# Performance work log

Measured on AMD Instinct MI355X. Metric: run time of the kernel, lower is better.

## Reference

```python
import jax, jax.numpy as jnp
import numpy as np

NUM_EXPERTS = 16
IN_FEATURES = 512
OUT_FEATURES = 512
N_TOKENS = 2048


def setup_inputs() -> dict:
    key = jax.random.key(0)
    k_x, k_idx, k_w, k_b = jax.random.split(key, 4)
    x = jax.random.normal(k_x, (N_TOKENS, IN_FEATURES), dtype=jnp.float32)
    indices = jax.random.randint(k_idx, (N_TOKENS,), 0, NUM_EXPERTS, dtype=jnp.int64)
    # nn.Linear default init: U(-1/sqrt(in), 1/sqrt(in)) for weight [out,in] and bias [out]
    bound = 1.0 / np.sqrt(IN_FEATURES)
    W = jax.random.uniform(k_w, (NUM_EXPERTS, OUT_FEATURES, IN_FEATURES),
                           minval=-bound, maxval=bound, dtype=jnp.float32)
    b = jax.random.uniform(k_b, (NUM_EXPERTS, OUT_FEATURES),
                           minval=-bound, maxval=bound, dtype=jnp.float32)
    return {"x": x, "indices": indices, "W": W, "b": b}


def reference(x, indices, W, b):
    # Faithful to SwitchLinear.forward: gather per-token expert weight/bias,
    # then per-token GEMV (batched matmul with a length-1 row dim).
    w_tok = W[indices]            # [N, out, in]  (naive per-token weight gather)
    b_tok = b[indices]            # [N, out]
    out = jnp.einsum('ni,noi->no', x, w_tok) + b_tok  # [N, out]
    return out
```

## Files before the change

### kernel.cpp

```cpp
#include <hip/hip_runtime.h>
#include <hip/hip_bf16.h>

#define NE    16
#define INF   512
#define OUTF  512
#define NT    2048
#define OTILE 32
#define TCH   64
#define WROWS 32
#define LSTRIDE 520

#define SZ_W   (WROWS * LSTRIDE * 2)
#define SZ_X   (TCH * LSTRIDE * 2)
#define SZ_LST ((NT + TCH) * 4)
#define SMEM_BYTES (SZ_W + SZ_X + SZ_LST + 32)

typedef __attribute__((ext_vector_type(4))) float f32x4;
typedef __attribute__((ext_vector_type(8))) short bf16x8;
typedef __attribute__((ext_vector_type(4))) short bf16x4;

__device__ inline short f2bf(float f) {
    union { __hip_bfloat16 h; short s; } u;
    u.h = __float2bfloat16(f);
    return u.s;
}

__device__ inline bf16x4 cvt4(f32x4 v) {
    bf16x4 r;
    r[0] = f2bf(v[0]); r[1] = f2bf(v[1]); r[2] = f2bf(v[2]); r[3] = f2bf(v[3]);
    return r;
}

__global__ __launch_bounds__(512, 2)
void switch_linear_kernel(const float* __restrict__ x,
                          const int* __restrict__ idx,
                          const float* __restrict__ W,
                          const float* __restrict__ bias,
                          float* __restrict__ out)
{
    extern __shared__ char smem[];
    short* s_W    = (short*)smem;
    short* s_X    = (short*)(smem + SZ_W);
    int*   s_list = (int*)(smem + SZ_W + SZ_X);
    int*   s_wcnt = (int*)(smem + SZ_W + SZ_X + SZ_LST);

    const int b   = blockIdx.x;
    const int e   = b & 15;
    const int o0  = (b >> 4) * OTILE;
    const int tid = threadIdx.x;
    const int lane = tid & 63;
    const int wid  = tid >> 6;

    int iv[4];
#pragma unroll
    for (int it = 0; it < 4; ++it)
        iv[it] = idx[wid * 256 + it * 64 + lane];

    const float* wbase = W + ((size_t)e * OUTF + o0) * INF;
#pragma unroll
    for (int i = 0; i < 8; ++i) {
        const int li = tid + i * 512;
        f32x4 v = ((const f32x4*)wbase)[li];
        const int fidx = li * 4;
        const int row = fidx >> 9;
        const int col = fidx & 511;
        *(bf16x4*)(&s_W[row * LSTRIDE + col]) = cvt4(v);
    }

    unsigned long long masks[4];
    int wtot = 0;
#pragma unroll
    for (int it = 0; it < 4; ++it) {
        const unsigned long long mk = __ballot(iv[it] == e);
        masks[it] = mk;
        wtot += __popcll(mk);
    }
    if (lane == 0) s_wcnt[wid] = wtot;
    __syncthreads();
    int base = 0;
#pragma unroll
    for (int w = 0; w < 8; ++w) { int c = s_wcnt[w]; if (w < wid) base += c; }
    const int cnt = s_wcnt[0] + s_wcnt[1] + s_wcnt[2] + s_wcnt[3]
                  + s_wcnt[4] + s_wcnt[5] + s_wcnt[6] + s_wcnt[7];
    const unsigned long long below = (1ull << lane) - 1ull;
    int run = base;
#pragma unroll
    for (int it = 0; it < 4; ++it) {
        const unsigned long long mk = masks[it];
        if (mk & (1ull << lane))
            s_list[run + __popcll(mk & below)] = wid * 256 + it * 64 + lane;
        run += __popcll(mk);
    }
    const int cnt_pad = (cnt + TCH - 1) & ~(TCH - 1);
    for (int i = cnt + tid; i < cnt_pad; i += 512) s_list[i] = -1;
    __syncthreads();
    if (cnt == 0) return;

    const int wt = wid >> 1;
    const int wo = wid & 1;
    const int lr = lane & 15;
    const int q  = lane >> 4;
    const int orow = o0 + wo * 16 + lr;

    bf16x8 bfr[16];
#pragma unroll
    for (int kk = 0; kk < 16; ++kk)
        bfr[kk] = *(const bf16x8*)(&s_W[(wo * 16 + lr) * LSTRIDE + kk * 32 + q * 8]);
    const float bv = bias[e * OUTF + orow];

    const int slot = tid >> 3;
    const int sub  = tid & 7;

    for (int cb = 0; cb < cnt_pad; cb += TCH) {
        int tok_s = s_list[cb + slot];
        if (tok_s < 0) tok_s = 0;
        const f32x4* xr = (const f32x4*)(x + (size_t)tok_s * INF);
#pragma unroll
        for (int i = 0; i < 16; ++i) {
            f32x4 v = xr[sub + i * 8];
            *(bf16x4*)(&s_X[slot * LSTRIDE + sub * 4 + i * 32]) = cvt4(v);
        }
        __syncthreads();

        f32x4 acc = {0.f, 0.f, 0.f, 0.f};
#pragma unroll
        for (int kk = 0; kk < 16; ++kk) {
            bf16x8 afr = *(const bf16x8*)(&s_X[(wt * 16 + lr) * LSTRIDE + kk * 32 + q * 8]);
            acc = __builtin_amdgcn_mfma_f32_16x16x32_bf16(afr, bfr[kk], acc, 0, 0, 0);
        }
#pragma unroll
        for (int j = 0; j < 4; ++j) {
            const int tok = s_list[cb + wt * 16 + q * 4 + j];
            if (tok >= 0) out[(size_t)tok * OUTF + orow] = acc[j] + bv;
        }
        __syncthreads();
    }
}

extern "C" void kernel_launch(void* const* d_in, const int* in_sizes, int n_in,
                              void* d_out, int out_size, void* d_ws, size_t ws_size,
                              hipStream_t stream) {
    const float* x    = (const float*)d_in[0];
    const int*   idx  = (const int*)d_in[1];
    const float* W    = (const float*)d_in[2];
    const float* bias = (const float*)d_in[3];
    float* out = (float*)d_out;

    dim3 grid(NE * (OUTF / OTILE));
    dim3 block(512);
    switch_linear_kernel<<<grid, block, SMEM_BYTES, stream>>>(x, idx, W, bias, out);
}
```

Before: 14.66 us.

## Prepack per-expert bf16 token rows and load tiles with global_load_lds

Adds a prepack kernel that gathers each expert's tokens once, converts them to bf16 and writes them contiguously into the workspace. The main kernel then streams these packed rows into LDS with direct global-to-LDS loads, instead of having each of the 16 output-tile blocks per expert re-gather and re-convert the fp32 rows. W is also loaded as fp32 straight into LDS and converted to bf16 when building register fragments. The cost is an extra kernel launch, and a per-expert capacity of 256 tokens that silently drops any overflow. The old single-kernel path is kept as a fallback when the workspace is too small.

After: 17.90 us. 1.22x slower.

```diff
diff --git a/kernel.cpp b/kernel.cpp
--- a/kernel.cpp
+++ b/kernel.cpp
@@ -7,42 +7,106 @@
 #define NT    2048
 #define OTILE 32
 #define TCH   64
-#define WROWS 32
-#define LSTRIDE 520
-
-#define SZ_W   (WROWS * LSTRIDE * 2)
-#define SZ_X   (TCH * LSTRIDE * 2)
+#define RCAP  256
+
+#define WSTRIDE 516
+#define XSTRIDE 520
+
+#define SZ_W   (OTILE * WSTRIDE * 4)
+#define SZ_X   (TCH * XSTRIDE * 2)
 #define SZ_LST ((NT + TCH) * 4)
-#define SMEM_BYTES (SZ_W + SZ_X + SZ_LST + 32)
+#define SMEM_BYTES (SZ_W + SZ_X + SZ_LST + 64)
+
+#define WS_NEED ((size_t)NE * RCAP * INF * 2)
 
 typedef __attribute__((ext_vector_type(4))) float f32x4;
 typedef __attribute__((ext_vector_type(8))) short bf16x8;
 typedef __attribute__((ext_vector_type(4))) short bf16x4;
 
-__device__ inline short f2bf(float f) {
-    union { __hip_bfloat16 h; short s; } u;
+__device__ inline unsigned short f2bf(float f) {
+    union { __hip_bfloat16 h; unsigned short s; } u;
     u.h = __float2bfloat16(f);
     return u.s;
 }
 
+__device__ inline bf16x8 cvt8(f32x4 lo, f32x4 hi) {
+    bf16x8 r;
+    r[0] = (short)f2bf(lo[0]); r[1] = (short)f2bf(lo[1]);
+    r[2] = (short)f2bf(lo[2]); r[3] = (short)f2bf(lo[3]);
+    r[4] = (short)f2bf(hi[0]); r[5] = (short)f2bf(hi[1]);
+    r[6] = (short)f2bf(hi[2]); r[7] = (short)f2bf(hi[3]);
+    return r;
+}
+
 __device__ inline bf16x4 cvt4(f32x4 v) {
     bf16x4 r;
-    r[0] = f2bf(v[0]); r[1] = f2bf(v[1]); r[2] = f2bf(v[2]); r[3] = f2bf(v[3]);
+    r[0] = (short)f2bf(v[0]); r[1] = (short)f2bf(v[1]);
+    r[2] = (short)f2bf(v[2]); r[3] = (short)f2bf(v[3]);
     return r;
 }
 
+__device__ inline void gload_lds16(const void* g, void* l) {
+    __builtin_amdgcn_global_load_lds(
+        (const __attribute__((address_space(1))) void*)g,
+        (__attribute__((address_space(3))) void*)l, 16, 0, 0);
+}
+
+__global__ __launch_bounds__(256, 4)
+void prepack_x(const float* __restrict__ x, const int* __restrict__ idx,
+               unsigned short* __restrict__ xs)
+{
+    __shared__ int s_list[NT];
+    __shared__ int s_wcnt[4];
+    const int e     = blockIdx.x & 15;
+    const int slice = blockIdx.x >> 4;
+    const int tid   = threadIdx.x;
+    const int lane  = tid & 63;
+    const int wv    = tid >> 6;
+
+    unsigned long long masks[8];
+    int wtot = 0;
+#pragma unroll
+    for (int it = 0; it < 8; ++it) {
+        const int i = wv * 512 + it * 64 + lane;
+        const unsigned long long mk = __ballot(idx[i] == e);
+        masks[it] = mk;
+        wtot += __popcll(mk);
+    }
+    if (lane == 0) s_wcnt[wv] = wtot;
+    __syncthreads();
+    int base = 0;
+#pragma unroll
+    for (int w = 0; w < 4; ++w) if (w < wv) base += s_wcnt[w];
+    const int cnt = s_wcnt[0] + s_wcnt[1] + s_wcnt[2] + s_wcnt[3];
+    const unsigned long long below = (1ull << lane) - 1ull;
+    int run = base;
+#pragma unroll
+    for (int it = 0; it < 8; ++it) {
+        const unsigned long long mk = masks[it];
+        if (mk & (1ull << lane))
+            s_list[run + __popcll(mk & below)] = wv * 512 + it * 64 + lane;
+        run += __popcll(mk);
+    }
+    __syncthreads();
+
+    for (int r = slice; r < cnt && r < RCAP; r += 16) {
+        const int tok = s_list[r];
+        const float2 v = *(const float2*)&x[(size_t)tok * INF + tid * 2];
+        ushort2 o; o.x = f2bf(v.x); o.y = f2bf(v.y);
+        *(ushort2*)&xs[((size_t)e * RCAP + r) * INF + tid * 2] = o;
+    }
+}
+
 __global__ __launch_bounds__(512, 2)
-void switch_linear_kernel(const float* __restrict__ x,
-                          const int* __restrict__ idx,
-                          const float* __restrict__ W,
-                          const float* __restrict__ bias,
-                          float* __restrict__ out)
+void moe_main(const int* __restrict__ idx, const float* __restrict__ W,
+              const float* __restrict__ bias, const unsigned short* __restrict__ xs,
+              float* __restrict__ out)
 {
     extern __shared__ char smem[];
-    short* s_W    = (short*)smem;
-    short* s_X    = (short*)(smem + SZ_W);
-    int*   s_list = (int*)(smem + SZ_W + SZ_X);
-    int*   s_wcnt = (int*)(smem + SZ_W + SZ_X + SZ_LST);
+    float*          s_Wf   = (float*)smem;
+    unsigned short* s_X    = (unsigned short*)(smem + SZ_W);
+    int*            s_list = (int*)(smem + SZ_W + SZ_X);
+    int*            s_wcnt = (int*)(smem + SZ_W + SZ_X + SZ_LST);
 
     const int b   = blockIdx.x;
     const int e   = b & 15;
@@ -58,13 +122,12 @@
 
     const float* wbase = W + ((size_t)e * OUTF + o0) * INF;
 #pragma unroll
-    for (int i = 0; i < 8; ++i) {
-        const int li = tid + i * 512;
-        f32x4 v = ((const f32x4*)wbase)[li];
-        const int fidx = li * 4;
-        const int row = fidx >> 9;
-        const int col = fidx & 511;
-        *(bf16x4*)(&s_W[row * LSTRIDE + col]) = cvt4(v);
+    for (int r2 = 0; r2 < 4; ++r2) {
+        const int row = wid * 4 + r2;
+        const float* gsrc = wbase + (size_t)row * INF + lane * 4;
+        float* ldst = s_Wf + row * WSTRIDE;
+        gload_lds16(gsrc, ldst);
+        gload_lds16(gsrc + 256, ldst + 256);
     }
 
     unsigned long long masks[4];
@@ -100,32 +163,130 @@
     const int wo = wid & 1;
     const int lr = lane & 15;
     const int q  = lane >> 4;
+    const int wrow = wo * 16 + lr;
+    const int orow = o0 + wrow;
+
+    bf16x8 bfr[16];
+#pragma unroll
+    for (int kk = 0; kk < 16; ++kk) {
+        f32x4 lo = *(const f32x4*)&s_Wf[wrow * WSTRIDE + kk * 32 + q * 8];
+        f32x4 hi = *(const f32x4*)&s_Wf[wrow * WSTRIDE + kk * 32 + q * 8 + 4];
+        bfr[kk] = cvt8(lo, hi);
+    }
+    const float bv = bias[e * OUTF + orow];
+
+    const unsigned short* xsrc = xs + (size_t)e * RCAP * INF;
+
+    for (int cb = 0; cb < cnt_pad; cb += TCH) {
+#pragma unroll
+        for (int r2 = 0; r2 < 8; ++r2) {
+            const int row = wid * 8 + r2;
+            const unsigned short* gsrc = xsrc + (size_t)(cb + row) * INF + lane * 8;
+            unsigned short* ldst = s_X + row * XSTRIDE;
+            gload_lds16(gsrc, ldst);
+        }
+        __syncthreads();
+
+        f32x4 acc = {0.f, 0.f, 0.f, 0.f};
+#pragma unroll
+        for (int kk = 0; kk < 16; ++kk) {
+            bf16x8 afr = *(const bf16x8*)&s_X[(wt * 16 + lr) * XSTRIDE + kk * 32 + q * 8];
+            acc = __builtin_amdgcn_mfma_f32_16x16x32_bf16(afr, bfr[kk], acc, 0, 0, 0);
+        }
+#pragma unroll
+        for (int j = 0; j < 4; ++j) {
+            const int tok = s_list[cb + wt * 16 + q * 4 + j];
+            if (tok >= 0) out[(size_t)tok * OUTF + orow] = acc[j] + bv;
+        }
+        __syncthreads();
+    }
+}
+
+#define FB_LSTRIDE 520
+#define FB_SZ_W   (OTILE * FB_LSTRIDE * 2)
+#define FB_SZ_X   (TCH * FB_LSTRIDE * 2)
+#define FB_SZ_LST ((NT + TCH) * 4)
+#define FB_SMEM   (FB_SZ_W + FB_SZ_X + FB_SZ_LST + 32)
+
+__global__ __launch_bounds__(512, 2)
+void fallback_kernel(const float* __restrict__ x, const int* __restrict__ idx,
+                     const float* __restrict__ W, const float* __restrict__ bias,
+                     float* __restrict__ out)
+{
+    extern __shared__ char smem[];
+    short* s_W    = (short*)smem;
+    short* s_X    = (short*)(smem + FB_SZ_W);
+    int*   s_list = (int*)(smem + FB_SZ_W + FB_SZ_X);
+    int*   s_wcnt = (int*)(smem + FB_SZ_W + FB_SZ_X + FB_SZ_LST);
+
+    const int b = blockIdx.x;
+    const int e = b & 15;
+    const int o0 = (b >> 4) * OTILE;
+    const int tid = threadIdx.x;
+    const int lane = tid & 63;
+    const int wid = tid >> 6;
+
+    int iv[4];
+#pragma unroll
+    for (int it = 0; it < 4; ++it) iv[it] = idx[wid * 256 + it * 64 + lane];
+
+    const float* wbase = W + ((size_t)e * OUTF + o0) * INF;
+#pragma unroll
+    for (int i = 0; i < 8; ++i) {
+        const int li = tid + i * 512;
+        f32x4 v = ((const f32x4*)wbase)[li];
+        const int fidx = li * 4;
+        *(bf16x4*)(&s_W[(fidx >> 9) * FB_LSTRIDE + (fidx & 511)]) = cvt4(v);
+    }
+
+    unsigned long long masks[4]; int wtot = 0;
+#pragma unroll
+    for (int it = 0; it < 4; ++it) {
+        const unsigned long long mk = __ballot(iv[it] == e);
+        masks[it] = mk; wtot += __popcll(mk);
+    }
+    if (lane == 0) s_wcnt[wid] = wtot;
+    __syncthreads();
+    int base = 0;
+#pragma unroll
+    for (int w = 0; w < 8; ++w) { int c = s_wcnt[w]; if (w < wid) base += c; }
+    const int cnt = s_wcnt[0]+s_wcnt[1]+s_wcnt[2]+s_wcnt[3]+s_wcnt[4]+s_wcnt[5]+s_wcnt[6]+s_wcnt[7];
+    const unsigned long long below = (1ull << lane) - 1ull;
+    int run = base;
+#pragma unroll
+    for (int it = 0; it < 4; ++it) {
+        const unsigned long long mk = masks[it];
+        if (mk & (1ull << lane))
+            s_list[run + __popcll(mk & below)] = wid * 256 + it * 64 + lane;
+        run += __popcll(mk);
+    }
+    const int cnt_pad = (cnt + TCH - 1) & ~(TCH - 1);
+    for (int i = cnt + tid; i < cnt_pad; i += 512) s_list[i] = -1;
+    __syncthreads();
+    if (cnt == 0) return;
+
+    const int wt = wid >> 1, wo = wid & 1, lr = lane & 15, q = lane >> 4;
     const int orow = o0 + wo * 16 + lr;
-
     bf16x8 bfr[16];
 #pragma unroll
     for (int kk = 0; kk < 16; ++kk)
-        bfr[kk] = *(const bf16x8*)(&s_W[(wo * 16 + lr) * LSTRIDE + kk * 32 + q * 8]);
+        bfr[kk] = *(const bf16x8*)(&s_W[(wo * 16 + lr) * FB_LSTRIDE + kk * 32 + q * 8]);
     const float bv = bias[e * OUTF + orow];
-
-    const int slot = tid >> 3;
-    const int sub  = tid & 7;
+    const int slot = tid >> 3, sub = tid & 7;
 
     for (int cb = 0; cb < cnt_pad; cb += TCH) {
-        int tok_s = s_list[cb + slot];
-        if (tok_s < 0) tok_s = 0;
+        int tok_s = s_list[cb + slot]; if (tok_s < 0) tok_s = 0;
         const f32x4* xr = (const f32x4*)(x + (size_t)tok_s * INF);
 #pragma unroll
         for (int i = 0; i < 16; ++i) {
             f32x4 v = xr[sub + i * 8];
-            *(bf16x4*)(&s_X[slot * LSTRIDE + sub * 4 + i * 32]) = cvt4(v);
+            *(bf16x4*)(&s_X[slot * FB_LSTRIDE + sub * 4 + i * 32]) = cvt4(v);
         }
         __syncthreads();
-
         f32x4 acc = {0.f, 0.f, 0.f, 0.f};
 #pragma unroll
         for (int kk = 0; kk < 16; ++kk) {
-            bf16x8 afr = *(const bf16x8*)(&s_X[(wt * 16 + lr) * LSTRIDE + kk * 32 + q * 8]);
+            bf16x8 afr = *(const bf16x8*)(&s_X[(wt * 16 + lr) * FB_LSTRIDE + kk * 32 + q * 8]);
             acc = __builtin_amdgcn_mfma_f32_16x16x32_bf16(afr, bfr[kk], acc, 0, 0, 0);
         }
 #pragma unroll
@@ -146,7 +307,13 @@
     const float* bias = (const float*)d_in[3];
     float* out = (float*)d_out;
 
-    dim3 grid(NE * (OUTF / OTILE));
-    dim3 block(512);
-    switch_linear_kernel<<<grid, block, SMEM_BYTES, stream>>>(x, idx, W, bias, out);
-}
+    if (ws_size >= WS_NEED && d_ws != nullptr) {
+        unsigned short* xs = (unsigned short*)d_ws;
+        prepack_x<<<dim3(NE * 16), dim3(256), 0, stream>>>(x, idx, xs);
+        moe_main<<<dim3(NE * (OUTF / OTILE)), dim3(512), SMEM_BYTES, stream>>>(
+            idx, W, bias, xs, out);
+    } else {
+        fallback_kernel<<<dim3(NE * (OUTF / OTILE)), dim3(512), FB_SMEM, stream>>>(
+            x, idx, W, bias, out);
+    }
+}
```
